# Performance work log

Measured on AMD Instinct MI355X. Metric: run time of the kernel, lower is better.

## Reference

```python
import jax, jax.numpy as jnp
import numpy as np
import math

# ---- hyperparameters (init_kwargs) ----
D = 2              # spatial dimension
MTOT = 65          # quadrature nodes per dimension (odd)
LENGTHSCALE = 0.1  # SE kernel lengthscale
OUTPUTSCALE = 1.0  # SE kernel variance
SIGMASQ = 0.05     # observation noise variance
CG_ITERS = 30      # fixed CG iteration count (replaces tol-based early stopping)
N_TRAIN = 100000
N_TEST = 50000
TWO_PI = 2.0 * math.pi


def setup_inputs() -> dict:
    key = jax.random.key(0)
    k1, k2, k3 = jax.random.split(key, 3)
    x = jax.random.uniform(k1, (N_TRAIN, D), dtype=jnp.float32)
    y = jax.random.normal(k2, (N_TRAIN,), dtype=jnp.float32)
    x_new = jax.random.uniform(k3, (N_TEST, D), dtype=jnp.float32)
    return {"x": x, "y": y, "x_new": x_new}


def _phases(col, h, freqs, isign):
    # exp(isign * i * 2*pi*h * x * k), shape [N, K]
    return jnp.exp((1j * isign * TWO_PI) * (h * col[:, None] * freqs[None, :]).astype(jnp.float32))


def _nudft_type1(pts, c, h, freqs):
    # fk[a,b] = sum_n c_n exp(-2*pi*i*h*(k_a x_n0 + k_b x_n1)); separable tensor grid
    E0 = _phases(pts[:, 0], h, freqs, -1.0)
    E1 = _phases(pts[:, 1], h, freqs, -1.0)
    return jnp.einsum('n,na,nb->ab', c.astype(jnp.complex64), E0, E1)


def _nudft_type2(pts, fk, h, freqs):
    # f_n = sum_{a,b} fk[a,b] exp(+2*pi*i*h*(k_a x_n0 + k_b x_n1))
    E0 = _phases(pts[:, 0], h, freqs, +1.0)
    E1 = _phases(pts[:, 1], h, freqs, +1.0)
    return jnp.einsum('ab,na,nb->n', fk, E0, E1)


def _cg(A, b, iters):
    # complex Hermitian-PSD conjugate gradients, fixed iteration count
    x0 = jnp.zeros_like(b)
    r0 = b
    rs0 = jnp.real(jnp.vdot(r0, r0))

    def step(carry, _):
        xk, r, p, rs = carry
        Ap = A(p)
        alpha = rs / jnp.real(jnp.vdot(p, Ap))
        xk = xk + alpha * p
        r = r - alpha * Ap
        rs_new = jnp.real(jnp.vdot(r, r))
        p = r + (rs_new / rs) * p
        return (xk, r, p, rs_new), None

    (xk, _, _, _), _ = jax.lax.scan(step, (x0, r0, r0, rs0), None, length=iters)
    return xk


def _forward(x, y, x_new):
    m = (MTOT - 1) // 2
    # geometry / quadrature (get_xis): domain extent L, spacing h = 1/L, grid k = -m..m
    x_all = jnp.concatenate((x, x_new), axis=0)
    L = jnp.max(jnp.max(x_all, axis=0) - jnp.min(x_all, axis=0))
    L = jnp.where(L <= 1e-9, jnp.float32(1.0), L)
    h = (1.0 / L).astype(jnp.float32)
    k = (jnp.arange(MTOT) - m).astype(jnp.float32)
    xis_1d = h * k
    X0, X1 = jnp.meshgrid(xis_1d, xis_1d, indexing='ij')
    sq = X0 * X0 + X1 * X1  # [MTOT, MTOT] squared frequency norm
    # squared-exponential spectral density S(s) = sigma_f^2 (2*pi*l^2)^(d/2) exp(-2*pi^2*l^2 |s|^2)
    l2 = LENGTHSCALE * LENGTHSCALE
    spec = OUTPUTSCALE * (TWO_PI * l2) ** (D / 2) * jnp.exp((-2.0 * math.pi ** 2 * l2) * sq)
    ws = jnp.sqrt(spec * h ** D).reshape(-1).astype(jnp.complex64)  # [M]

    # rhs = ws * F^H y  (type-1 NUFFT, exact NUDFT)
    rhs = ws * _nudft_type1(x, y, h, k).reshape(-1)

    # Toeplitz convolution vector v[o] = sum_n exp(-2*pi*i*h*o.x_n), offsets -(mtot-1)..(mtot-1)
    kk = (jnp.arange(2 * MTOT - 1) - (MTOT - 1)).astype(jnp.float32)
    Ev0 = _phases(x[:, 0], h, kk, -1.0)
    Ev1 = _phases(x[:, 1], h, kk, -1.0)
    v = jnp.einsum('na,nb->ab', Ev0, Ev1)  # [2M-1, 2M-1]
    # circularly align offset 0 to index 0, precompute FFT
    v_circ = jnp.roll(v, shift=(-(MTOT - 1), -(MTOT - 1)), axis=(0, 1))
    vhat = jnp.fft.fftn(v_circ)
    s_fft = (2 * MTOT - 1, 2 * MTOT - 1)

    def toeplitz_apply(w):  # w: [MTOT, MTOT] complex
        W = jnp.fft.fftn(w, s=s_fft)
        full = jnp.fft.ifftn(vhat * W)
        return full[:MTOT, :MTOT]

    def A_mean(beta):  # (W F^H F W + sigma^2 I) beta, beta flat [M]
        wb = (ws * beta).reshape(MTOT, MTOT)
        Tw = toeplitz_apply(wb).reshape(-1)
        return ws * Tw + SIGMASQ * beta

    beta = _cg(A_mean, rhs, CG_ITERS)
    # posterior mean at test points via type-2 NUFFT
    yhat = jnp.real(_nudft_type2(x_new, (ws * beta).reshape(MTOT, MTOT), h, k))
    return yhat


def reference(x, y, x_new):
    return _forward(x, y, x_new)
```

## Files before the change

### kernel.cpp

```cpp
#include <hip/hip_runtime.h>
#include <math.h>

#define M2 4225
#define NTRAIN 100000
#define NTEST 50000
#define CGITERS 30
#define TWO_PI_D 6.283185307179586476925287
#define TPI32 6.28318530717958647692f

#define F_H 0
#define F_RS 1
#define F_PAP 2
#define F_RSN 3
#define F_WS 8
#define F_RHS 4234
#define F_X 12684
#define F_R 21134
#define F_P 29584
#define F_AP 38034
#define F_PB 46484
#define F_VF 50710
#define F_VHAT 83992
#define F_PROD 117274
#define D_VPART 125330
#define D_FKPART 2271890

#define NCHUNK 128
#define PTSB2 782
#define VHALF 8385
#define VH2 16770
#define FKHALF 2145
#define FH2 4290

__device__ __forceinline__ unsigned fkey(float f){
  unsigned u = __float_as_uint(f);
  return (u & 0x80000000u) ? ~u : (u | 0x80000000u);
}
__device__ __forceinline__ float fdec(unsigned k){
  unsigned u = (k & 0x80000000u) ? (k & 0x7fffffffu) : ~k;
  return __uint_as_float(u);
}

__global__ void k_init(unsigned* mm){
  if (threadIdx.x == 0){
    mm[0] = 0xFFFFFFFFu; mm[1] = 0u; mm[2] = 0xFFFFFFFFu; mm[3] = 0u;
  }
}

__global__ void k_minmax(const float* __restrict__ x, const float* __restrict__ xn,
                         unsigned* __restrict__ mm){
  int tid = blockIdx.x * blockDim.x + threadIdx.x;
  int str = gridDim.x * blockDim.x;
  float mn0 = 1e30f, mx0 = -1e30f, mn1 = 1e30f, mx1 = -1e30f;
  const float2* a = (const float2*)x;
  for (int i = tid; i < NTRAIN; i += str){
    float2 v = a[i];
    mn0 = fminf(mn0, v.x); mx0 = fmaxf(mx0, v.x);
    mn1 = fminf(mn1, v.y); mx1 = fmaxf(mx1, v.y);
  }
  const float2* b = (const float2*)xn;
  for (int i = tid; i < NTEST; i += str){
    float2 v = b[i];
    mn0 = fminf(mn0, v.x); mx0 = fmaxf(mx0, v.x);
    mn1 = fminf(mn1, v.y); mx1 = fmaxf(mx1, v.y);
  }
  for (int off = 32; off; off >>= 1){
    mn0 = fminf(mn0, __shfl_xor(mn0, off, 64));
    mx0 = fmaxf(mx0, __shfl_xor(mx0, off, 64));
    mn1 = fminf(mn1, __shfl_xor(mn1, off, 64));
    mx1 = fmaxf(mx1, __shfl_xor(mx1, off, 64));
  }
  if ((threadIdx.x & 63) == 0){
    atomicMin(&mm[0], fkey(mn0)); atomicMax(&mm[1], fkey(mx0));
    atomicMin(&mm[2], fkey(mn1)); atomicMax(&mm[3], fkey(mx1));
  }
}

__global__ void k_setup(float* __restrict__ wsf){
  const unsigned* mm = (const unsigned*)(wsf + 4);
  float mn0 = fdec(mm[0]), mx0 = fdec(mm[1]);
  float mn1 = fdec(mm[2]), mx1 = fdec(mm[3]);
  float d0 = __fsub_rn(mx0, mn0), d1 = __fsub_rn(mx1, mn1);
  float L = fmaxf(d0, d1);
  if (L <= 1e-9f) L = 1.0f;
  float hf = __fdiv_rn(1.0f, L);
  if (threadIdx.x == 0) wsf[F_H] = hf;
  const float c0f = (float)(TWO_PI_D * 0.01);
  const float c1f = (float)(-2.0 * 9.869604401089358618834 * 0.01);
  float h2f = __fmul_rn(hf, hf);
  for (int e = threadIdx.x; e < M2; e += blockDim.x){
    int r = e / 65, c = e - r * 65;
    float xi0 = __fmul_rn(hf, (float)(r - 32));
    float xi1 = __fmul_rn(hf, (float)(c - 32));
    float sq = __fadd_rn(__fmul_rn(xi0, xi0), __fmul_rn(xi1, xi1));
    float spec = __fmul_rn(c0f, expf(__fmul_rn(c1f, sq)));
    wsf[F_WS + e] = sqrtf(__fmul_rn(spec, h2f));
  }
}

__launch_bounds__(256, 1)
__global__ void k_v_main(const float* __restrict__ x, const float* __restrict__ wsf,
                         double* __restrict__ vpart){
  __shared__ float2 aL[16][80];
  __shared__ float2 bL[16][80];
  __shared__ float hxs[16][2];
  const float hf = wsf[F_H];
  const int tid = threadIdx.x;
  const int t0 = tid >> 4, t1 = tid & 15;
  const int colbase = blockIdx.y * 65;
  const int ncol = blockIdx.y ? 64 : 65;
  double2 acc[5][5];
  #pragma unroll
  for (int k = 0; k < 5; ++k)
    #pragma unroll
    for (int m = 0; m < 5; ++m) acc[k][m] = make_double2(0.0, 0.0);
  const int p0 = blockIdx.x * PTSB2;
  const int pend = min(p0 + PTSB2, NTRAIN);
  for (int base = p0; base < pend; base += 16){
    if (tid < 32){
      int p = tid >> 1, d = tid & 1;
      int gp = base + p;
      hxs[p][d] = (gp < pend) ? __fmul_rn(hf, x[2 * gp + d]) : 0.f;
    }
    __syncthreads();
    for (int i = tid; i < 16 * 80; i += 256){
      int p = i / 80;
      int o = i - p * 80;
      int gp = base + p;
      float2 va = make_float2(0.f, 0.f);
      float2 vb = make_float2(0.f, 0.f);
      if (gp < pend){
        if (o < 65){
          float t = __fmul_rn(hxs[p][0], (float)o);
          float sn, cs; sincosf(__fmul_rn(TPI32, t), &sn, &cs);
          va = make_float2(cs, -sn);
        }
        if (o < ncol){
          float t = __fmul_rn(hxs[p][1], (float)(colbase + o - 64));
          float sn, cs; sincosf(__fmul_rn(TPI32, t), &sn, &cs);
          vb = make_float2(cs, -sn);
        }
      }
      aL[p][o] = va;
      bL[p][o] = vb;
    }
    __syncthreads();
    #pragma unroll 1
    for (int p = 0; p < 16; ++p){
      float2 av[5], bv[5];
      #pragma unroll
      for (int k = 0; k < 5; ++k) av[k] = aL[p][t0 + 16 * k];
      #pragma unroll
      for (int m = 0; m < 5; ++m) bv[m] = bL[p][t1 + 16 * m];
      #pragma unroll
      for (int k = 0; k < 5; ++k)
        #pragma unroll
        for (int m = 0; m < 5; ++m){
          acc[k][m].x += (double)av[k].x * (double)bv[m].x - (double)av[k].y * (double)bv[m].y;
          acc[k][m].y += (double)av[k].x * (double)bv[m].y + (double)av[k].y * (double)bv[m].x;
        }
    }
    __syncthreads();
  }
  double* outp = vpart + (size_t)blockIdx.x * VH2;
  #pragma unroll
  for (int k = 0; k < 5; ++k){
    int o0 = t0 + 16 * k;
    if (o0 < 65){
      #pragma unroll
      for (int m = 0; m < 5; ++m){
        int jl = t1 + 16 * m;
        if (jl < ncol){
          int e = o0 * 129 + colbase + jl;
          outp[2 * e] = acc[k][m].x;
          outp[2 * e + 1] = acc[k][m].y;
        }
      }
    }
  }
}

__launch_bounds__(256, 1)
__global__ void k_fk_main(const float* __restrict__ x, const float* __restrict__ y,
                          const float* __restrict__ wsf, double* __restrict__ fkpart){
  __shared__ float2 aL[16][48];
  __shared__ float2 bL[16][80];
  __shared__ float hxs[16][2];
  __shared__ float ys[16];
  const float hf = wsf[F_H];
  const int tid = threadIdx.x;
  const int t0 = tid >> 4, t1 = tid & 15;
  double2 acc[3][5];
  #pragma unroll
  for (int k = 0; k < 3; ++k)
    #pragma unroll
    for (int m = 0; m < 5; ++m) acc[k][m] = make_double2(0.0, 0.0);
  const int p0 = blockIdx.x * PTSB2;
  const int pend = min(p0 + PTSB2, NTRAIN);
  for (int base = p0; base < pend; base += 16){
    if (tid < 32){
      int p = tid >> 1, d = tid & 1;
      int gp = base + p;
      hxs[p][d] = (gp < pend) ? __fmul_rn(hf, x[2 * gp + d]) : 0.f;
    } else if (tid < 48){
      int p = tid - 32;
      int gp = base + p;
      ys[p] = (gp < pend) ? y[gp] : 0.f;
    }
    __syncthreads();
    for (int i = tid; i < 16 * 48; i += 256){
      int p = i / 48, o = i - p * 48;
      int gp = base + p;
      float2 val = make_float2(0.f, 0.f);
      if (o < 33 && gp < pend){
        float t = __fmul_rn(hxs[p][0], (float)o);
        float sn, cs; sincosf(__fmul_rn(TPI32, t), &sn, &cs);
        val = make_float2(__fmul_rn(ys[p], cs), __fmul_rn(ys[p], -sn));
      }
      aL[p][o] = val;
    }
    for (int i = tid; i < 16 * 80; i += 256){
      int p = i / 80, j = i - p * 80;
      int gp = base + p;
      float2 val = make_float2(0.f, 0.f);
      if (j < 65 && gp < pend){
        float t = __fmul_rn(hxs[p][1], (float)(j - 32));
        float sn, cs; sincosf(__fmul_rn(TPI32, t), &sn, &cs);
        val = make_float2(cs, -sn);
      }
      bL[p][j] = val;
    }
    __syncthreads();
    #pragma unroll 1
    for (int p = 0; p < 16; ++p){
      float2 av[3], bv[5];
      #pragma unroll
      for (int k = 0; k < 3; ++k) av[k] = aL[p][t0 + 16 * k];
      #pragma unroll
      for (int m = 0; m < 5; ++m) bv[m] = bL[p][t1 + 16 * m];
      #pragma unroll
      for (int k = 0; k < 3; ++k)
        #pragma unroll
        for (int m = 0; m < 5; ++m){
          acc[k][m].x += (double)av[k].x * (double)bv[m].x - (double)av[k].y * (double)bv[m].y;
          acc[k][m].y += (double)av[k].x * (double)bv[m].y + (double)av[k].y * (double)bv[m].x;
        }
    }
    __syncthreads();
  }
  double* outp = fkpart + (size_t)blockIdx.x * FH2;
  #pragma unroll
  for (int k = 0; k < 3; ++k){
    int o0 = t0 + 16 * k;
    if (o0 < 33){
      #pragma unroll
      for (int m = 0; m < 5; ++m){
        int j = t1 + 16 * m;
        if (j < 65){
          int e = o0 * 65 + j;
          outp[2 * e] = acc[k][m].x;
          outp[2 * e + 1] = acc[k][m].y;
        }
      }
    }
  }
}

__global__ void k_reduce_v(const double* __restrict__ wsd, float* __restrict__ wsf){
  int e = blockIdx.x * blockDim.x + threadIdx.x;
  if (e >= VHALF) return;
  const double* vp = wsd + D_VPART;
  double sr = 0.0, si = 0.0;
  for (int k = 0; k < NCHUNK; ++k){
    sr += vp[(size_t)k * VH2 + 2 * e];
    si += vp[(size_t)k * VH2 + 2 * e + 1];
  }
  float r32 = (float)sr, i32 = (float)si;
  int o0 = e / 129, j = e - o0 * 129;
  float2* vF = (float2*)(wsf + F_VF);
  vF[(o0 + 64) * 129 + j] = make_float2(r32, i32);
  if (o0 > 0) vF[(64 - o0) * 129 + (128 - j)] = make_float2(r32, -i32);
}

__global__ void k_reduce_fk(const double* __restrict__ wsd, float* __restrict__ wsf){
  int e = blockIdx.x * blockDim.x + threadIdx.x;
  if (e >= FKHALF) return;
  const double* fp = wsd + D_FKPART;
  double sr = 0.0, si = 0.0;
  for (int k = 0; k < NCHUNK; ++k){
    sr += fp[(size_t)k * FH2 + 2 * e];
    si += fp[(size_t)k * FH2 + 2 * e + 1];
  }
  float fr = (float)sr, fi = (float)si;
  int a = e / 65, c = e - a * 65;
  int ef = (a + 32) * 65 + c;
  float wf = wsf[F_WS + ef];
  float* rhs = wsf + F_RHS;
  rhs[2 * ef] = __fmul_rn(wf, fr);
  rhs[2 * ef + 1] = __fmul_rn(wf, fi);
  if (a > 0){
    int ef2 = (32 - a) * 65 + (64 - c);
    float wf2 = wsf[F_WS + ef2];
    rhs[2 * ef2] = __fmul_rn(wf2, fr);
    rhs[2 * ef2 + 1] = -__fmul_rn(wf2, fi);
  }
}

__launch_bounds__(192)
__global__ void k_vhat(float* __restrict__ wsf){
  __shared__ double twc[129], tws[129];
  __shared__ double t1r[129], t1i[129];
  int p = blockIdx.x, t = threadIdx.x;
  if (t < 129){
    double ang = TWO_PI_D * (double)t / 129.0;
    double s, c; sincos(ang, &s, &c);
    twc[t] = c; tws[t] = s;
  }
  __syncthreads();
  if (t < 129){
    const float2* vF = (const float2*)(wsf + F_VF);
    int n = t;
    int nsrc = (n + 64) % 129;
    double ar = 0.0, ai = 0.0;
    for (int m = 0; m < 129; ++m){
      float2 v = vF[((m + 64) % 129) * 129 + nsrc];
      int idx = (p * m) % 129;
      double wr = twc[idx], wi = -tws[idx];
      ar += (double)v.x * wr - (double)v.y * wi;
      ai += (double)v.x * wi + (double)v.y * wr;
    }
    t1r[n] = ar; t1i[n] = ai;
  }
  __syncthreads();
  if (t < 129){
    int q = t;
    double ar = 0.0, ai = 0.0;
    for (int n = 0; n < 129; ++n){
      int idx = (q * n) % 129;
      double wr = twc[idx], wi = -tws[idx];
      ar += t1r[n] * wr - t1i[n] * wi;
      ai += t1r[n] * wi + t1i[n] * wr;
    }
    ((float2*)(wsf + F_VHAT))[p * 129 + q] = make_float2((float)ar, (float)ai);
  }
}

__global__ void k_cg_init(float* __restrict__ wsf){
  int e = blockIdx.x * blockDim.x + threadIdx.x;
  if (e >= M2) return;
  const float2* rhs = (const float2*)(wsf + F_RHS);
  float2 b = rhs[e];
  ((float2*)(wsf + F_X))[e] = make_float2(0.f, 0.f);
  ((float2*)(wsf + F_R))[e] = b;
  ((float2*)(wsf + F_P))[e] = b;
  wsf[F_PB + e] = __fadd_rn(__fmul_rn(b.x, b.x), __fmul_rn(b.y, b.y));
}

__device__ __forceinline__ float pw_leaf(const float* d, int o, int n){
  float r0 = d[o], r1 = d[o+1], r2 = d[o+2], r3 = d[o+3];
  float r4 = d[o+4], r5 = d[o+5], r6 = d[o+6], r7 = d[o+7];
  int i = 8;
  int lim = n - (n & 7);
  for (; i < lim; i += 8){
    r0 = __fadd_rn(r0, d[o+i]);   r1 = __fadd_rn(r1, d[o+i+1]);
    r2 = __fadd_rn(r2, d[o+i+2]); r3 = __fadd_rn(r3, d[o+i+3]);
    r4 = __fadd_rn(r4, d[o+i+4]); r5 = __fadd_rn(r5, d[o+i+5]);
    r6 = __fadd_rn(r6, d[o+i+6]); r7 = __fadd_rn(r7, d[o+i+7]);
  }
  float res = __fadd_rn(__fadd_rn(__fadd_rn(r0, r1), __fadd_rn(r2, r3)),
                        __fadd_rn(__fadd_rn(r4, r5), __fadd_rn(r6, r7)));
  for (; i < n; ++i) res = __fadd_rn(res, d[o+i]);
  return res;
}

__device__ __forceinline__ void pw_tree(const float* pb, float* T, int tid){
  if (tid < 16){
    const int tb[16] = {0,264,528,792,1056,1320,1584,1848,
                        2112,2376,2640,2904,3168,3432,3696,3960};
    int base = tb[tid];
    int sz3 = (tid == 15) ? 73 : 72;
    float L0 = pw_leaf(pb, base, 128);
    float L1 = pw_leaf(pb, base + 128, 64);
    float L2 = pw_leaf(pb, base + 192, sz3);
    T[tid] = __fadd_rn(L0, __fadd_rn(L1, L2));
  }
  __syncthreads();
  if (tid == 0){
    float s0 = __fadd_rn(__fadd_rn(T[0], T[1]), __fadd_rn(T[2], T[3]));
    float s1 = __fadd_rn(__fadd_rn(T[4], T[5]), __fadd_rn(T[6], T[7]));
    float s2 = __fadd_rn(__fadd_rn(T[8], T[9]), __fadd_rn(T[10], T[11]));
    float s3 = __fadd_rn(__fadd_rn(T[12], T[13]), __fadd_rn(T[14], T[15]));
    T[0] = __fadd_rn(__fadd_rn(s0, s1), __fadd_rn(s2, s3));
  }
}

__launch_bounds__(256)
__global__ void k_pair0(float* __restrict__ wsf){
  __shared__ float pb[M2];
  __shared__ float T[16];
  int tid = threadIdx.x;
  for (int i = tid; i < M2; i += 256) pb[i] = wsf[F_PB + i];
  __syncthreads();
  pw_tree(pb, T, tid);
  __syncthreads();
  if (tid == 0) wsf[F_RS] = T[0];
}

__launch_bounds__(192)
__global__ void k_wfft(float* __restrict__ wsf){
  __shared__ double twc[129], tws[129];
  __shared__ double t1r[65], t1i[65];
  int pr = blockIdx.x, t = threadIdx.x;
  if (t < 129){
    double ang = TWO_PI_D * (double)t / 129.0;
    double s, c; sincos(ang, &s, &c);
    twc[t] = c; tws[t] = s;
  }
  __syncthreads();
  if (t < 65){
    const float2* P = (const float2*)(wsf + F_P);
    const float* W = wsf + F_WS;
    int n = t;
    double ar = 0.0, ai = 0.0;
    for (int m = 0; m < 65; ++m){
      int e = m * 65 + n;
      float2 p = P[e];
      float w = W[e];
      float wbr = __fmul_rn(w, p.x), wbi = __fmul_rn(w, p.y);
      int idx = (pr * m) % 129;
      double wr = twc[idx], wi = -tws[idx];
      ar += (double)wbr * wr - (double)wbi * wi;
      ai += (double)wbr * wi + (double)wbi * wr;
    }
    t1r[n] = ar; t1i[n] = ai;
  }
  __syncthreads();
  if (t < 129){
    int q = t;
    double ar = 0.0, ai = 0.0;
    for (int n = 0; n < 65; ++n){
      int idx = (q * n) % 129;
      double wr = twc[idx], wi = -tws[idx];
      ar += t1r[n] * wr - t1i[n] * wi;
      ai += t1r[n] * wi + t1i[n] * wr;
    }
    float Wr = (float)ar, Wi = (float)ai;
    float2 v = ((const float2*)(wsf + F_VHAT))[pr * 129 + q];
    float prre = __fsub_rn(__fmul_rn(v.x, Wr), __fmul_rn(v.y, Wi));
    float prim = __fadd_rn(__fmul_rn(v.x, Wi), __fmul_rn(v.y, Wr));
    ((float2*)(wsf + F_PROD))[pr * 129 + q] = make_float2(prre, prim);
  }
}

__launch_bounds__(192)
__global__ void k_ifft(float* __restrict__ wsf){
  __shared__ double twc[129], tws[129];
  __shared__ double ur[129], ui[129];
  int m = blockIdx.x, t = threadIdx.x;
  if (t < 129){
    double ang = TWO_PI_D * (double)t / 129.0;
    double s, c; sincos(ang, &s, &c);
    twc[t] = c; tws[t] = s;
  }
  __syncthreads();
  if (t < 129){
    const float2* prod = (const float2*)(wsf + F_PROD);
    int q = t;
    double ar = 0.0, ai = 0.0;
    for (int pr = 0; pr < 129; ++pr){
      float2 v = prod[pr * 129 + q];
      int idx = (m * pr) % 129;
      double wr = twc[idx], wi = tws[idx];
      ar += (double)v.x * wr - (double)v.y * wi;
      ai += (double)v.x * wi + (double)v.y * wr;
    }
    const double sc = 1.0 / 129.0;
    ur[q] = ar * sc; ui[q] = ai * sc;
  }
  __syncthreads();
  if (t < 65){
    int n = t;
    double ar = 0.0, ai = 0.0;
    for (int q = 0; q < 129; ++q){
      int idx = (n * q) % 129;
      double wr = twc[idx], wi = tws[idx];
      ar += ur[q] * wr - ui[q] * wi;
      ai += ur[q] * wi + ui[q] * wr;
    }
    const double sc = 1.0 / 129.0;
    float Twr = (float)(ar * sc), Twi = (float)(ai * sc);
    int e = m * 65 + n;
    float w = wsf[F_WS + e];
    float2 p = ((const float2*)(wsf + F_P))[e];
    float Apx = __fadd_rn(__fmul_rn(w, Twr), __fmul_rn(0.05f, p.x));
    float Apy = __fadd_rn(__fmul_rn(w, Twi), __fmul_rn(0.05f, p.y));
    ((float2*)(wsf + F_AP))[e] = make_float2(Apx, Apy);
    wsf[F_PB + e] = __fadd_rn(__fmul_rn(p.x, Apx), __fmul_rn(p.y, Apy));
  }
}

__launch_bounds__(256)
__global__ void k_cgstep(float* __restrict__ wsf){
  __shared__ float pb[M2];
  __shared__ float T[16];
  __shared__ float sh[2];
  int tid = threadIdx.x;
  for (int i = tid; i < M2; i += 256) pb[i] = wsf[F_PB + i];
  __syncthreads();
  pw_tree(pb, T, tid);
  __syncthreads();
  if (tid == 0){
    float rs = wsf[F_RS];
    sh[1] = rs;
    sh[0] = __fdiv_rn(rs, T[0]);
  }
  __syncthreads();
  float alpha = sh[0];
  float2* X = (float2*)(wsf + F_X);
  float2* R = (float2*)(wsf + F_R);
  float2* P = (float2*)(wsf + F_P);
  const float2* AP = (const float2*)(wsf + F_AP);
  for (int e = tid; e < M2; e += 256){
    float2 p = P[e], ap = AP[e], xv = X[e], rv = R[e];
    xv.x = __fadd_rn(xv.x, __fmul_rn(alpha, p.x));
    xv.y = __fadd_rn(xv.y, __fmul_rn(alpha, p.y));
    rv.x = __fsub_rn(rv.x, __fmul_rn(alpha, ap.x));
    rv.y = __fsub_rn(rv.y, __fmul_rn(alpha, ap.y));
    X[e] = xv; R[e] = rv;
    pb[e] = __fadd_rn(__fmul_rn(rv.x, rv.x), __fmul_rn(rv.y, rv.y));
  }
  __syncthreads();
  pw_tree(pb, T, tid);
  __syncthreads();
  if (tid == 0){
    float rsn = T[0];
    sh[0] = __fdiv_rn(rsn, sh[1]);
    wsf[F_RS] = rsn;
  }
  __syncthreads();
  float beta = sh[0];
  for (int e = tid; e < M2; e += 256){
    float2 rv = R[e], p = P[e];
    P[e] = make_float2(__fadd_rn(rv.x, __fmul_rn(beta, p.x)),
                       __fadd_rn(rv.y, __fmul_rn(beta, p.y)));
  }
}

__launch_bounds__(256)
__global__ void k_predict(const float* __restrict__ xn, const float* __restrict__ wsf,
                          float* __restrict__ out){
  __shared__ double fbRe[M2];
  __shared__ double fbIm[M2];
  const float hf = wsf[F_H];
  const float* wsq = wsf + F_WS;
  const float2* xb = (const float2*)(wsf + F_X);
  int tid = threadIdx.x;
  for (int i = tid; i < M2; i += 256){
    float w = wsq[i]; float2 q = xb[i];
    fbRe[i] = (double)__fmul_rn(w, q.x);
    fbIm[i] = (double)__fmul_rn(w, q.y);
  }
  __syncthreads();
  int lane = tid & 63;
  int wid = (blockIdx.x * 256 + tid) >> 6;
  int nw = (gridDim.x * 256) >> 6;
  for (int n = wid; n < NTEST; n += nw){
    float hx0 = __fmul_rn(hf, xn[2 * n]);
    float hx1 = __fmul_rn(hf, xn[2 * n + 1]);
    float t0 = __fmul_rn(hx0, (float)(lane - 32));
    float s0, c0; sincosf(__fmul_rn(TPI32, t0), &s0, &c0);
    float t1 = __fmul_rn(hx1, (float)(lane - 32));
    float s1, c1; sincosf(__fmul_rn(TPI32, t1), &s1, &c1);
    float t0x = __fmul_rn(hx0, 32.0f);
    float s0x, c0x; sincosf(__fmul_rn(TPI32, t0x), &s0x, &c0x);
    float t1x = __fmul_rn(hx1, 32.0f);
    float s1x, c1x; sincosf(__fmul_rn(TPI32, t1x), &s1x, &c1x);
    double e0r = (double)c0, e0i = (double)s0;
    double e1r = (double)c1, e1i = (double)s1;
    double gr = 0.0, gi = 0.0;
    for (int a = 0; a < 64; ++a){
      double er = __shfl(e0r, a, 64);
      double ei = __shfl(e0i, a, 64);
      double fr = fbRe[a * 65 + lane];
      double fi = fbIm[a * 65 + lane];
      gr += fr * er - fi * ei;
      gi += fr * ei + fi * er;
    }
    {
      double fr = fbRe[64 * 65 + lane], fi = fbIm[64 * 65 + lane];
      gr += fr * (double)c0x - fi * (double)s0x;
      gi += fr * (double)s0x + fi * (double)c0x;
    }
    double contrib = gr * e1r - gi * e1i;
    {
      double fr = fbRe[lane * 65 + 64], fi = fbIm[lane * 65 + 64];
      double ur = fr * e0r - fi * e0i;
      double ui = fr * e0i + fi * e0r;
      contrib += ur * (double)c1x - ui * (double)s1x;
      if (lane == 0){
        double fr2 = fbRe[64 * 65 + 64], fi2 = fbIm[64 * 65 + 64];
        double vr = fr2 * (double)c0x - fi2 * (double)s0x;
        double vi = fr2 * (double)s0x + fi2 * (double)c0x;
        contrib += vr * (double)c1x - vi * (double)s1x;
      }
    }
    for (int off = 32; off; off >>= 1) contrib += __shfl_xor(contrib, off, 64);
    if (lane == 0) out[n] = (float)contrib;
  }
}

extern "C" void kernel_launch(void* const* d_in, const int* in_sizes, int n_in,
                              void* d_out, int out_size, void* d_ws, size_t ws_size,
                              hipStream_t stream){
  const float* x = (const float*)d_in[0];
  const float* y = (const float*)d_in[1];
  const float* xnew = (const float*)d_in[2];
  float* wsf = (float*)d_ws;
  double* wsd = (double*)d_ws;
  float* out = (float*)d_out;
  unsigned* mm = (unsigned*)(wsf + 4);

  k_init<<<1, 64, 0, stream>>>(mm);
  k_minmax<<<256, 256, 0, stream>>>(x, xnew, mm);
  k_setup<<<1, 256, 0, stream>>>(wsf);
  k_v_main<<<dim3(NCHUNK, 2), 256, 0, stream>>>(x, wsf, wsd + D_VPART);
  k_fk_main<<<NCHUNK, 256, 0, stream>>>(x, y, wsf, wsd + D_FKPART);
  k_reduce_v<<<33, 256, 0, stream>>>(wsd, wsf);
  k_reduce_fk<<<9, 256, 0, stream>>>(wsd, wsf);
  k_vhat<<<129, 192, 0, stream>>>(wsf);
  k_cg_init<<<17, 256, 0, stream>>>(wsf);
  k_pair0<<<1, 256, 0, stream>>>(wsf);
  for (int it = 0; it < CGITERS; ++it){
    k_wfft<<<129, 192, 0, stream>>>(wsf);
    k_ifft<<<65, 192, 0, stream>>>(wsf);
    k_cgstep<<<1, 256, 0, stream>>>(wsf);
  }
  k_predict<<<256, 256, 0, stream>>>(xnew, wsf, out);
}
```

Measured before the change: 2.426 ms.

## Split NUDFT accumulation columns across more blocks with one column per thread

The v and fk accumulation kernels now split the column dimension across 9 and 5 grid blocks. Each thread owns a single column with 5 or 3 double accumulators, replacing the 5x5 and 3x5 register tiles. This raises block count and occupancy and relaxes the launch bounds, at the cost of recomputing the row phase tables (aL sincos) in every column block and losing register reuse of the B values.

```diff
diff --git a/kernel.cpp b/kernel.cpp
--- a/kernel.cpp
+++ b/kernel.cpp
@@ -98,22 +98,19 @@
   }
 }
 
-__launch_bounds__(256, 1)
+__launch_bounds__(256)
 __global__ void k_v_main(const float* __restrict__ x, const float* __restrict__ wsf,
                          double* __restrict__ vpart){
   __shared__ float2 aL[16][80];
-  __shared__ float2 bL[16][80];
+  __shared__ float2 bL[16][16];
   __shared__ float hxs[16][2];
   const float hf = wsf[F_H];
   const int tid = threadIdx.x;
   const int t0 = tid >> 4, t1 = tid & 15;
-  const int colbase = blockIdx.y * 65;
-  const int ncol = blockIdx.y ? 64 : 65;
-  double2 acc[5][5];
+  const int jcol = blockIdx.y * 16 + t1;
+  double2 acc[5];
   #pragma unroll
-  for (int k = 0; k < 5; ++k)
-    #pragma unroll
-    for (int m = 0; m < 5; ++m) acc[k][m] = make_double2(0.0, 0.0);
+  for (int k = 0; k < 5; ++k) acc[k] = make_double2(0.0, 0.0);
   const int p0 = blockIdx.x * PTSB2;
   const int pend = min(p0 + PTSB2, NTRAIN);
   for (int base = p0; base < pend; base += 16){
@@ -128,73 +125,68 @@
       int o = i - p * 80;
       int gp = base + p;
       float2 va = make_float2(0.f, 0.f);
+      if (gp < pend && o < 65){
+        float t = __fmul_rn(hxs[p][0], (float)o);
+        float sn, cs; sincosf(__fmul_rn(TPI32, t), &sn, &cs);
+        va = make_float2(cs, -sn);
+      }
+      aL[p][o] = va;
+    }
+    {
+      int p = t0, c = t1;
+      int gp = base + p;
+      int j = blockIdx.y * 16 + c;
       float2 vb = make_float2(0.f, 0.f);
-      if (gp < pend){
-        if (o < 65){
-          float t = __fmul_rn(hxs[p][0], (float)o);
-          float sn, cs; sincosf(__fmul_rn(TPI32, t), &sn, &cs);
-          va = make_float2(cs, -sn);
-        }
-        if (o < ncol){
-          float t = __fmul_rn(hxs[p][1], (float)(colbase + o - 64));
-          float sn, cs; sincosf(__fmul_rn(TPI32, t), &sn, &cs);
-          vb = make_float2(cs, -sn);
-        }
-      }
-      aL[p][o] = va;
-      bL[p][o] = vb;
+      if (gp < pend && j < 129){
+        float t = __fmul_rn(hxs[p][1], (float)(j - 64));
+        float sn, cs; sincosf(__fmul_rn(TPI32, t), &sn, &cs);
+        vb = make_float2(cs, -sn);
+      }
+      bL[p][c] = vb;
     }
     __syncthreads();
     #pragma unroll 1
     for (int p = 0; p < 16; ++p){
-      float2 av[5], bv[5];
+      float2 bv = bL[p][t1];
+      float2 av[5];
       #pragma unroll
       for (int k = 0; k < 5; ++k) av[k] = aL[p][t0 + 16 * k];
       #pragma unroll
-      for (int m = 0; m < 5; ++m) bv[m] = bL[p][t1 + 16 * m];
-      #pragma unroll
-      for (int k = 0; k < 5; ++k)
-        #pragma unroll
-        for (int m = 0; m < 5; ++m){
-          acc[k][m].x += (double)av[k].x * (double)bv[m].x - (double)av[k].y * (double)bv[m].y;
-          acc[k][m].y += (double)av[k].x * (double)bv[m].y + (double)av[k].y * (double)bv[m].x;
-        }
+      for (int k = 0; k < 5; ++k){
+        acc[k].x += (double)av[k].x * (double)bv.x - (double)av[k].y * (double)bv.y;
+        acc[k].y += (double)av[k].x * (double)bv.y + (double)av[k].y * (double)bv.x;
+      }
     }
     __syncthreads();
   }
   double* outp = vpart + (size_t)blockIdx.x * VH2;
-  #pragma unroll
-  for (int k = 0; k < 5; ++k){
-    int o0 = t0 + 16 * k;
-    if (o0 < 65){
-      #pragma unroll
-      for (int m = 0; m < 5; ++m){
-        int jl = t1 + 16 * m;
-        if (jl < ncol){
-          int e = o0 * 129 + colbase + jl;
-          outp[2 * e] = acc[k][m].x;
-          outp[2 * e + 1] = acc[k][m].y;
-        }
-      }
-    }
-  }
-}
-
-__launch_bounds__(256, 1)
+  if (jcol < 129){
+    #pragma unroll
+    for (int k = 0; k < 5; ++k){
+      int o0 = t0 + 16 * k;
+      if (o0 < 65){
+        int e = o0 * 129 + jcol;
+        outp[2 * e] = acc[k].x;
+        outp[2 * e + 1] = acc[k].y;
+      }
+    }
+  }
+}
+
+__launch_bounds__(256)
 __global__ void k_fk_main(const float* __restrict__ x, const float* __restrict__ y,
                           const float* __restrict__ wsf, double* __restrict__ fkpart){
   __shared__ float2 aL[16][48];
-  __shared__ float2 bL[16][80];
+  __shared__ float2 bL[16][16];
   __shared__ float hxs[16][2];
   __shared__ float ys[16];
   const float hf = wsf[F_H];
   const int tid = threadIdx.x;
   const int t0 = tid >> 4, t1 = tid & 15;
-  double2 acc[3][5];
+  const int jcol = blockIdx.y * 16 + t1;
+  double2 acc[3];
   #pragma unroll
-  for (int k = 0; k < 3; ++k)
-    #pragma unroll
-    for (int m = 0; m < 5; ++m) acc[k][m] = make_double2(0.0, 0.0);
+  for (int k = 0; k < 3; ++k) acc[k] = make_double2(0.0, 0.0);
   const int p0 = blockIdx.x * PTSB2;
   const int pend = min(p0 + PTSB2, NTRAIN);
   for (int base = p0; base < pend; base += 16){
@@ -219,48 +211,42 @@
       }
       aL[p][o] = val;
     }
-    for (int i = tid; i < 16 * 80; i += 256){
-      int p = i / 80, j = i - p * 80;
+    {
+      int p = t0, c = t1;
       int gp = base + p;
-      float2 val = make_float2(0.f, 0.f);
-      if (j < 65 && gp < pend){
+      int j = blockIdx.y * 16 + c;
+      float2 vb = make_float2(0.f, 0.f);
+      if (gp < pend && j < 65){
         float t = __fmul_rn(hxs[p][1], (float)(j - 32));
         float sn, cs; sincosf(__fmul_rn(TPI32, t), &sn, &cs);
-        val = make_float2(cs, -sn);
-      }
-      bL[p][j] = val;
+        vb = make_float2(cs, -sn);
+      }
+      bL[p][c] = vb;
     }
     __syncthreads();
     #pragma unroll 1
     for (int p = 0; p < 16; ++p){
-      float2 av[3], bv[5];
+      float2 bv = bL[p][t1];
+      float2 av[3];
       #pragma unroll
       for (int k = 0; k < 3; ++k) av[k] = aL[p][t0 + 16 * k];
       #pragma unroll
-      for (int m = 0; m < 5; ++m) bv[m] = bL[p][t1 + 16 * m];
-      #pragma unroll
-      for (int k = 0; k < 3; ++k)
-        #pragma unroll
-        for (int m = 0; m < 5; ++m){
-          acc[k][m].x += (double)av[k].x * (double)bv[m].x - (double)av[k].y * (double)bv[m].y;
-          acc[k][m].y += (double)av[k].x * (double)bv[m].y + (double)av[k].y * (double)bv[m].x;
-        }
+      for (int k = 0; k < 3; ++k){
+        acc[k].x += (double)av[k].x * (double)bv.x - (double)av[k].y * (double)bv.y;
+        acc[k].y += (double)av[k].x * (double)bv.y + (double)av[k].y * (double)bv.x;
+      }
     }
     __syncthreads();
   }
   double* outp = fkpart + (size_t)blockIdx.x * FH2;
-  #pragma unroll
-  for (int k = 0; k < 3; ++k){
-    int o0 = t0 + 16 * k;
-    if (o0 < 33){
-      #pragma unroll
-      for (int m = 0; m < 5; ++m){
-        int j = t1 + 16 * m;
-        if (j < 65){
-          int e = o0 * 65 + j;
-          outp[2 * e] = acc[k][m].x;
-          outp[2 * e + 1] = acc[k][m].y;
-        }
+  if (jcol < 65){
+    #pragma unroll
+    for (int k = 0; k < 3; ++k){
+      int o0 = t0 + 16 * k;
+      if (o0 < 33){
+        int e = o0 * 65 + jcol;
+        outp[2 * e] = acc[k].x;
+        outp[2 * e + 1] = acc[k].y;
       }
     }
   }
@@ -623,8 +609,8 @@
   k_init<<<1, 64, 0, stream>>>(mm);
   k_minmax<<<256, 256, 0, stream>>>(x, xnew, mm);
   k_setup<<<1, 256, 0, stream>>>(wsf);
-  k_v_main<<<dim3(NCHUNK, 2), 256, 0, stream>>>(x, wsf, wsd + D_VPART);
-  k_fk_main<<<NCHUNK, 256, 0, stream>>>(x, y, wsf, wsd + D_FKPART);
+  k_v_main<<<dim3(NCHUNK, 9), 256, 0, stream>>>(x, wsf, wsd + D_VPART);
+  k_fk_main<<<dim3(NCHUNK, 5), 256, 0, stream>>>(x, y, wsf, wsd + D_FKPART);
   k_reduce_v<<<33, 256, 0, stream>>>(wsd, wsf);
   k_reduce_fk<<<9, 256, 0, stream>>>(wsd, wsf);
   k_vhat<<<129, 192, 0, stream>>>(wsf);
```

Result: no change. 2.381 ms (-1.9%).
